# Optimization experiments

Hardware: AMD Instinct MI355X
Metric: run time of the kernel (lower is better)

## Reference

```python
import jax, jax.numpy as jnp
import numpy as np

B, T, D_MODEL = 4, 2048, 1024
D_EXPERT, N_EXPERTS, TOP_K = 4096, 8, 2
CAPACITY_FACTOR = 1.25
AUX_COEFF, Z_COEFF = 0.01, 0.001


def setup_inputs() -> dict:
    key = jax.random.key(0)
    k = jax.random.split(key, 4)
    x = jax.random.normal(k[0], (B, T, D_MODEL), jnp.float32)
    Wr = jax.random.normal(k[1], (D_MODEL, N_EXPERTS), jnp.float32) * 0.02
    W1 = jax.random.normal(k[2], (N_EXPERTS, D_MODEL, D_EXPERT), jnp.float32) * (1.0 / np.sqrt(D_MODEL))
    b1 = jnp.zeros((N_EXPERTS, D_EXPERT), jnp.float32)
    W2 = jax.random.normal(k[3], (N_EXPERTS, D_EXPERT, D_MODEL), jnp.float32) * (1.0 / np.sqrt(D_EXPERT))
    b2 = jnp.zeros((N_EXPERTS, D_MODEL), jnp.float32)
    return {"x": x, "Wr": Wr, "W1": W1, "b1": b1, "W2": W2, "b2": b2}


def reference(x, Wr, W1, b1, W2, b2):
    Bb, Tt, D = x.shape
    N = Bb * Tt
    E = W1.shape[0]
    capacity = max(1, int(N / E * CAPACITY_FACTOR * TOP_K))

    xf = x.reshape(N, D)
    logits = xf @ Wr                                    # (N, E)
    z_loss = jnp.mean(jax.nn.logsumexp(logits, axis=-1) ** 2)
    probs = jax.nn.softmax(logits, axis=-1)             # (N, E)

    topk_p, topk_i = jax.lax.top_k(probs, TOP_K)        # (N, K)
    # one-hot expert mask (top-k experts are distinct per token)
    mask = jnp.zeros((N, E), probs.dtype).at[jnp.arange(N)[:, None], topk_i].set(1.0)

    # capacity truncation: keep first `capacity` assigned tokens per expert, in token order
    pos = (jnp.cumsum(mask, axis=0) - mask).astype(jnp.int32)   # exclusive rank within expert
    keep = (pos < capacity) & (mask > 0)
    mask_t = jnp.where(keep, mask, jnp.zeros_like(mask))

    # Switch-style aux loss on truncated mask
    total_sel = jnp.maximum(mask_t.sum(), 1.0)
    f_i = mask_t.sum(axis=0) / total_sel
    P_i = probs.mean(axis=0)
    aux_loss = E * jnp.sum(f_i * P_i)

    # normalized top-k combine weights (differentiable through probs)
    tk_raw = jnp.take_along_axis(probs, topk_i, axis=1)          # (N, K)
    tk = tk_raw / jnp.maximum(tk_raw.sum(axis=-1, keepdims=True), 1e-9)

    # dispatch tokens into (E, capacity, D) buffer; dropped tokens scatter out of range
    pos_safe = jnp.where(keep, pos, capacity)                    # capacity -> dropped
    pos_k = jnp.take_along_axis(pos_safe, topk_i, axis=1)        # (N, K)
    upd = jnp.broadcast_to(xf[:, None, :], (N, TOP_K, D)).reshape(-1, D)
    buf = jnp.zeros((E, capacity, D), x.dtype).at[topk_i.reshape(-1), pos_k.reshape(-1)].set(upd, mode='drop')

    # grouped expert MLP
    h = jax.nn.relu(jnp.einsum('ecd,edf->ecf', buf, W1) + b1[:, None, :])
    eo = jnp.einsum('ecf,efd->ecd', h, W2) + b2[:, None, :]      # (E, capacity, D)

    # combine: gather each token's top-k expert outputs, weight, sum; dropped -> weight 0
    valid_k = jnp.take_along_axis(keep, topk_i, axis=1)          # (N, K) bool
    w = tk * valid_k.astype(tk.dtype)
    pos_g = jnp.minimum(pos_k, capacity - 1)
    gathered = eo[topk_i, pos_g]                                 # (N, K, D)
    out = jnp.einsum('nk,nkd->nd', w, gathered).reshape(Bb, Tt, D)

    total_aux = AUX_COEFF * aux_loss + Z_COEFF * z_loss
    return out, aux_loss, z_loss, total_aux
```

## Files before the change

kernel.cpp:

```cpp
#include <hip/hip_runtime.h>
#include <stdint.h>

#define N_TOK    8192
#define DM       1024
#define DE       4096
#define NEXP     8
#define CAP      2560
#define AUX_CO   0.01f
#define Z_CO     0.001f

typedef __attribute__((ext_vector_type(4))) float f32x4;
typedef __attribute__((ext_vector_type(8))) __bf16 bf16x8;

static __device__ __forceinline__ unsigned short f2bf(float f) {
  union { float f; uint32_t u; } v; v.f = f;
  uint32_t r = 0x7fffu + ((v.u >> 16) & 1u);
  return (unsigned short)((v.u + r) >> 16);
}
static __device__ __forceinline__ float bf2f(unsigned short u) {
  union { uint32_t u; float f; } v; v.u = ((uint32_t)u) << 16;
  return v.f;
}

#define GLD16(g, l) __builtin_amdgcn_global_load_lds( \
    (const __attribute__((address_space(1))) void*)(g), \
    (__attribute__((address_space(3))) void*)(l), 16, 0, 0)

__global__ void init_inv(int* __restrict__ inv) {
  int i = blockIdx.x * 256 + threadIdx.x;
  if (i < NEXP * CAP) inv[i] = -1;
}

__global__ __launch_bounds__(256) void transpose_to_bf16(
    const float* __restrict__ in, unsigned short* __restrict__ out, int R, int C)
{
  __shared__ float tile[32][33];
  const size_t eoff = (size_t)blockIdx.z * R * C;
  const int bx = blockIdx.x * 32, by = blockIdx.y * 32;
  const int r = threadIdx.x >> 3, c4 = (threadIdx.x & 7) * 4;
  const float4 v = *(const float4*)&in[eoff + (size_t)(by + r) * C + bx + c4];
  tile[r][c4 + 0] = v.x; tile[r][c4 + 1] = v.y;
  tile[r][c4 + 2] = v.z; tile[r][c4 + 3] = v.w;
  __syncthreads();
  const int oc = threadIdx.x >> 3, r4 = (threadIdx.x & 7) * 4;
  ushort4 o;
  o.x = f2bf(tile[r4 + 0][oc]); o.y = f2bf(tile[r4 + 1][oc]);
  o.z = f2bf(tile[r4 + 2][oc]); o.w = f2bf(tile[r4 + 3][oc]);
  *(ushort4*)&out[eoff + (size_t)(bx + oc) * R + by + r4] = o;
}

__global__ __launch_bounds__(256) void router_kernel(
    const float* __restrict__ x, const float* __restrict__ Wr,
    int* __restrict__ topk, float* __restrict__ tkw, float* __restrict__ zP)
{
  const int tid = threadIdx.x, lane = tid & 63, wave = tid >> 6;
  float zacc = 0.f;
  float pacc[NEXP];
#pragma unroll
  for (int e = 0; e < NEXP; ++e) pacc[e] = 0.f;

  for (int it = 0; it < 4; ++it) {
    const int t = blockIdx.x * 16 + it * 4 + wave;
    float acc[NEXP];
#pragma unroll
    for (int e = 0; e < NEXP; ++e) acc[e] = 0.f;
    const f32x4* x4 = (const f32x4*)(x + (size_t)t * DM);
#pragma unroll
    for (int i = 0; i < 4; ++i) {
      f32x4 xv = x4[i * 64 + lane];
#pragma unroll
      for (int j = 0; j < 4; ++j) {
        const float xs = xv[j];
        const float* wr = Wr + (size_t)((i * 64 + lane) * 4 + j) * NEXP;
#pragma unroll
        for (int e = 0; e < NEXP; ++e) acc[e] += xs * wr[e];
      }
    }
#pragma unroll
    for (int m = 32; m; m >>= 1)
#pragma unroll
      for (int e = 0; e < NEXP; ++e) acc[e] += __shfl_xor(acc[e], m);

    float mx = acc[0];
#pragma unroll
    for (int e = 1; e < NEXP; ++e) mx = fmaxf(mx, acc[e]);
    float p[NEXP], s = 0.f;
#pragma unroll
    for (int e = 0; e < NEXP; ++e) { p[e] = expf(acc[e] - mx); s += p[e]; }
    const float lse = mx + logf(s);
    zacc += lse * lse;
    const float inv_s = 1.f / s;
#pragma unroll
    for (int e = 0; e < NEXP; ++e) pacc[e] += p[e] * inv_s;

    int e0 = 0; float v0 = p[0];
#pragma unroll
    for (int e = 1; e < NEXP; ++e) if (p[e] > v0) { v0 = p[e]; e0 = e; }
    int e1 = -1; float v1 = -1.f;
#pragma unroll
    for (int e = 0; e < NEXP; ++e) if (e != e0 && p[e] > v1) { v1 = p[e]; e1 = e; }

    const float pr0 = v0 * inv_s, pr1 = v1 * inv_s;
    const float denom = fmaxf(pr0 + pr1, 1e-9f);
    if (lane == 0) {
      topk[2*t]   = e0; topk[2*t+1] = e1;
      tkw[2*t]    = pr0 / denom; tkw[2*t+1] = pr1 / denom;
    }
  }
  __shared__ float blk[4][9];
  if (lane == 0) {
    blk[wave][0] = zacc;
#pragma unroll
    for (int e = 0; e < NEXP; ++e) blk[wave][1 + e] = pacc[e];
  }
  __syncthreads();
  if (tid < 9)
    zP[blockIdx.x * 9 + tid] = blk[0][tid] + blk[1][tid] + blk[2][tid] + blk[3][tid];
}

__global__ __launch_bounds__(512) void scan_kernel(
    const int2* __restrict__ topk, const float2* __restrict__ tkw,
    int* __restrict__ posk, float* __restrict__ wts,
    int* __restrict__ inv, int* __restrict__ kept)
{
  const int lane = threadIdx.x & 63;
  const int e = threadIdx.x >> 6;
  int base = 0;
  const uint64_t below = (lane == 63) ? 0xFFFFFFFFFFFFFFFFull >> 1
                                      : ((1ull << lane) - 1ull);
  for (int i = 0; i < N_TOK / 64; ++i) {
    const int t = i * 64 + lane;
    const int2 ti = topk[t];
    const float2 w = tkw[t];
    const bool hit = (ti.x == e) || (ti.y == e);
    const uint64_t m = __ballot(hit);
    if (hit) {
      const int pos = base + (int)__popcll(m & below);
      const bool kp = pos < CAP;
      const int k = (ti.x == e) ? 0 : 1;
      posk[2*t + k] = kp ? pos : CAP;
      wts[2*t + k]  = kp ? ((k == 0) ? w.x : w.y) : 0.f;
      if (kp) inv[e * CAP + pos] = t;
    }
    base += (int)__popcll(m);
  }
  if (lane == 0) kept[e] = base < CAP ? base : CAP;
}

__global__ __launch_bounds__(256) void dispatch_kernel(
    const float* __restrict__ x, const int* __restrict__ inv,
    unsigned short* __restrict__ buf)
{
  const int slot = blockIdx.x;
  const int t = inv[slot];
  ushort4 o;
  if (t >= 0) {
    const f32x4 v = ((const f32x4*)(x + (size_t)t * DM))[threadIdx.x];
    o.x = f2bf(v[0]); o.y = f2bf(v[1]); o.z = f2bf(v[2]); o.w = f2bf(v[3]);
  } else {
    o.x = 0; o.y = 0; o.z = 0; o.w = 0;
  }
  ((ushort4*)(buf + (size_t)slot * DM))[threadIdx.x] = o;
}

template<int BM, int BN, bool RELU>
__global__ __launch_bounds__(512, (BM == 256) ? 2 : 4) void gemm2p(
    const unsigned short* __restrict__ A,
    const unsigned short* __restrict__ Bt,
    const float* __restrict__ bias,
    unsigned short* __restrict__ C,
    const int* __restrict__ kept,
    int M, int N, int K, int mt, int nt, int nwg)
{
  constexpr int MF = BM / 32;
  constexpr int NF = BN / 64;
  constexpr int ABUF = BM * 64;
  constexpr int BBUF = BN * 64;
  __shared__ __attribute__((aligned(16))) unsigned short As[2 * ABUF];
  __shared__ __attribute__((aligned(16))) unsigned short Bs[2 * BBUF];

  const int tid = threadIdx.x, lane = tid & 63, wave = tid >> 6;
  const int wr = wave >> 2, wc = wave & 3;
  const int frow = lane & 15, kgrp = lane >> 4;

  int wg = (int)blockIdx.x;
  wg = (wg & 7) * (nwg >> 3) + (wg >> 3);
  const int ntpe = mt * nt;
  const int e = wg / ntpe, rr = wg % ntpe;
  const int m0 = (rr / nt) * BM;
  const int n0 = (rr % nt) * BN;
  if (m0 >= kept[e]) return;

  const unsigned short* Ae = A  + (size_t)e * M * K + (size_t)m0 * K;
  const unsigned short* Be = Bt + (size_t)e * N * K + (size_t)n0 * K;

  const int srow = tid >> 3;
  const int scol = ((tid & 7) ^ (srow & 7)) * 8;

  auto stage = [&](int buf, int k0) {
#pragma unroll
    for (int i = 0; i < BM / 64; ++i)
      GLD16(Ae + (size_t)(i * 64 + srow) * K + (k0 + scol),
            &As[buf * ABUF + i * 4096 + tid * 8]);
#pragma unroll
    for (int i = 0; i < BN / 64; ++i)
      GLD16(Be + (size_t)(i * 64 + srow) * K + (k0 + scol),
            &Bs[buf * BBUF + i * 4096 + tid * 8]);
  };

  f32x4 acc[MF][NF];
#pragma unroll
  for (int m = 0; m < MF; ++m)
#pragma unroll
    for (int n = 0; n < NF; ++n) acc[m][n] = (f32x4){0.f, 0.f, 0.f, 0.f};

  const int nk = K >> 6;
  stage(0, 0);
  for (int t = 0; t < nk; ++t) {
    const int cur = t & 1;
    __syncthreads();
    if (t + 1 < nk) stage(cur ^ 1, (t + 1) * 64);
#pragma unroll
    for (int kk = 0; kk < 2; ++kk) {
      bf16x8 bq[NF], af[MF];
#pragma unroll
      for (int n = 0; n < NF; ++n) {
        const int row = wc * (BN / 4) + n * 16 + frow;
        const int slot = (kk * 4 + kgrp) ^ (row & 7);
        bq[n] = *(const bf16x8*)&Bs[cur * BBUF + row * 64 + slot * 8];
      }
#pragma unroll
      for (int m = 0; m < MF; ++m) {
        const int row = wr * (BM / 2) + m * 16 + frow;
        const int slot = (kk * 4 + kgrp) ^ (row & 7);
        af[m] = *(const bf16x8*)&As[cur * ABUF + row * 64 + slot * 8];
      }
      __builtin_amdgcn_s_setprio(1);
#pragma unroll
      for (int m = 0; m < MF; ++m)
#pragma unroll
        for (int n = 0; n < NF; ++n)
          acc[m][n] = __builtin_amdgcn_mfma_f32_16x16x32_bf16(af[m], bq[n], acc[m][n], 0, 0, 0);
      __builtin_amdgcn_s_setprio(0);
    }
  }

  const int r0 = m0 + wr * (BM / 2) + 4 * kgrp;
  const int c0 = n0 + wc * (BN / 4) + frow;
#pragma unroll
  for (int n = 0; n < NF; ++n) {
    const int cc = c0 + n * 16;
    const float bv = bias[(size_t)e * N + cc];
#pragma unroll
    for (int m = 0; m < MF; ++m) {
#pragma unroll
      for (int r = 0; r < 4; ++r) {
        float v = acc[m][n][r] + bv;
        if (RELU) v = fmaxf(v, 0.f);
        C[((size_t)e * M + (r0 + m * 16 + r)) * N + cc] = f2bf(v);
      }
    }
  }
}

__global__ __launch_bounds__(256) void combine_kernel(
    const unsigned short* __restrict__ eo, const int* __restrict__ posk,
    const float* __restrict__ wts, const int* __restrict__ topk,
    float* __restrict__ out)
{
  const int t = blockIdx.x;
  const int e0 = topk[2*t], e1 = topk[2*t+1];
  int p0 = posk[2*t], p1 = posk[2*t+1];
  p0 = p0 < CAP - 1 ? p0 : CAP - 1;
  p1 = p1 < CAP - 1 ? p1 : CAP - 1;
  const float w0 = wts[2*t], w1 = wts[2*t+1];
  const ushort4 a = ((const ushort4*)(eo + ((size_t)e0 * CAP + p0) * DM))[threadIdx.x];
  const ushort4 b = ((const ushort4*)(eo + ((size_t)e1 * CAP + p1) * DM))[threadIdx.x];
  f32x4 o;
  o[0] = w0 * bf2f(a.x) + w1 * bf2f(b.x);
  o[1] = w0 * bf2f(a.y) + w1 * bf2f(b.y);
  o[2] = w0 * bf2f(a.z) + w1 * bf2f(b.z);
  o[3] = w0 * bf2f(a.w) + w1 * bf2f(b.w);
  ((f32x4*)(out + (size_t)t * DM))[threadIdx.x] = o;
}

__global__ __launch_bounds__(64) void finalize_kernel(
    const float* __restrict__ zP, const int* __restrict__ kept,
    float* __restrict__ outs)
{
  const int lane = threadIdx.x;
  float v[9];
#pragma unroll
  for (int e = 0; e < 9; ++e) {
    float s = 0.f;
    for (int b = 0; b < 8; ++b) s += zP[(lane * 8 + b) * 9 + e];
    v[e] = s;
  }
#pragma unroll
  for (int m = 32; m; m >>= 1)
#pragma unroll
    for (int e = 0; e < 9; ++e) v[e] += __shfl_xor(v[e], m);
  if (lane == 0) {
    const float z = v[0] / (float)N_TOK;
    float total = 0.f;
    for (int e = 0; e < NEXP; ++e) total += (float)kept[e];
    total = fmaxf(total, 1.f);
    float aux = 0.f;
    for (int e = 0; e < NEXP; ++e)
      aux += ((float)kept[e] / total) * (v[1 + e] / (float)N_TOK);
    aux *= (float)NEXP;
    outs[0] = aux;
    outs[1] = z;
    outs[2] = AUX_CO * aux + Z_CO * z;
  }
}

extern "C" void kernel_launch(void* const* d_in, const int* in_sizes, int n_in,
                              void* d_out, int out_size, void* d_ws, size_t ws_size,
                              hipStream_t stream)
{
  const float* x  = (const float*)d_in[0];
  const float* Wr = (const float*)d_in[1];
  const float* W1 = (const float*)d_in[2];
  const float* b1 = (const float*)d_in[3];
  const float* W2 = (const float*)d_in[4];
  const float* b2 = (const float*)d_in[5];
  float* out = (float*)d_out;

  char* p = (char*)d_ws;
  auto alloc = [&](size_t bytes) {
    char* q = p; p += (bytes + 255) & ~(size_t)255; return q;
  };
  unsigned short* W1t = (unsigned short*)alloc((size_t)NEXP * DM * DE * 2);
  unsigned short* W2t = (unsigned short*)alloc((size_t)NEXP * DM * DE * 2);
  unsigned short* buf = (unsigned short*)alloc((size_t)NEXP * CAP * DM * 2);
  unsigned short* h   = (unsigned short*)alloc((size_t)NEXP * CAP * DE * 2);
  unsigned short* eo  = (unsigned short*)alloc((size_t)NEXP * CAP * DM * 2);
  int*   topk = (int*)alloc((size_t)N_TOK * 2 * 4);
  float* tkw  = (float*)alloc((size_t)N_TOK * 2 * 4);
  int*   posk = (int*)alloc((size_t)N_TOK * 2 * 4);
  float* wts  = (float*)alloc((size_t)N_TOK * 2 * 4);
  int*   inv  = (int*)alloc((size_t)NEXP * CAP * 4);
  int*   kept = (int*)alloc((size_t)NEXP * 4);
  float* zP   = (float*)alloc((size_t)512 * 9 * 4);

  init_inv<<<(NEXP * CAP + 255) / 256, 256, 0, stream>>>(inv);
  transpose_to_bf16<<<dim3(DE / 32, DM / 32, NEXP), 256, 0, stream>>>(W1, W1t, DM, DE);
  transpose_to_bf16<<<dim3(DM / 32, DE / 32, NEXP), 256, 0, stream>>>(W2, W2t, DE, DM);
  router_kernel<<<512, 256, 0, stream>>>(x, Wr, topk, tkw, zP);
  scan_kernel<<<1, 512, 0, stream>>>((const int2*)topk, (const float2*)tkw, posk, wts, inv, kept);
  dispatch_kernel<<<NEXP * CAP, 256, 0, stream>>>(x, inv, buf);

  gemm2p<256, 256, true><<<1280, 512, 0, stream>>>(
      buf, W1t, b1, h, kept, CAP, DE, DM, 10, 16, 1280);
  gemm2p<128, 128, false><<<1280, 512, 0, stream>>>(
      h, W2t, b2, eo, kept, CAP, DM, DE, 20, 8, 1280);

  combine_kernel<<<N_TOK, 256, 0, stream>>>(eo, posk, wts, topk, out);
  finalize_kernel<<<1, 64, 0, stream>>>(zP, kept, out + (size_t)N_TOK * DM);
}
```

Before: 651.1 us.

## Add hand-scheduled 8-phase pipelined GEMM for first expert layer and fold inv init into scan

Replaces the first expert GEMM with a new 256x256 kernel that splits each K-step into four MFMA quadrants, interleaving LDS reads and async global-to-LDS loads between them with explicit waitcnt, barriers and priority hints. The aim is to overlap memory traffic with MFMA work more tightly. The scan kernel now stages topk and weights in shared memory and fills the unused inv slots itself, which removes the separate init kernel launch. The manual scheduling is fragile and depends on exact vmcnt counts being correct.

```diff
diff --git a/kernel.cpp b/kernel.cpp
--- a/kernel.cpp
+++ b/kernel.cpp
@@ -22,14 +22,15 @@
   return v.f;
 }
 
+#define MEMFENCE() asm volatile("" ::: "memory")
+#define BAR()    do { MEMFENCE(); __builtin_amdgcn_s_barrier(); MEMFENCE(); } while (0)
+#define LGKM0()  asm volatile("s_waitcnt lgkmcnt(0)" ::: "memory")
+#define LGKM8()  asm volatile("s_waitcnt lgkmcnt(8)" ::: "memory")
+#define VMW(N)   asm volatile("s_waitcnt vmcnt(" #N ")" ::: "memory")
+#define SB0()    __builtin_amdgcn_sched_barrier(0)
 #define GLD16(g, l) __builtin_amdgcn_global_load_lds( \
     (const __attribute__((address_space(1))) void*)(g), \
     (__attribute__((address_space(3))) void*)(l), 16, 0, 0)
-
-__global__ void init_inv(int* __restrict__ inv) {
-  int i = blockIdx.x * 256 + threadIdx.x;
-  if (i < NEXP * CAP) inv[i] = -1;
-}
 
 __global__ __launch_bounds__(256) void transpose_to_bf16(
     const float* __restrict__ in, unsigned short* __restrict__ out, int R, int C)
@@ -123,15 +124,21 @@
     int* __restrict__ posk, float* __restrict__ wts,
     int* __restrict__ inv, int* __restrict__ kept)
 {
-  const int lane = threadIdx.x & 63;
-  const int e = threadIdx.x >> 6;
+  __shared__ int2   stopk[N_TOK];
+  __shared__ float2 stkw[N_TOK];
+  const int tid = threadIdx.x;
+  for (int j = tid; j < N_TOK; j += 512) { stopk[j] = topk[j]; stkw[j] = tkw[j]; }
+  __syncthreads();
+
+  const int lane = tid & 63;
+  const int e = tid >> 6;
   int base = 0;
   const uint64_t below = (lane == 63) ? 0xFFFFFFFFFFFFFFFFull >> 1
                                       : ((1ull << lane) - 1ull);
   for (int i = 0; i < N_TOK / 64; ++i) {
     const int t = i * 64 + lane;
-    const int2 ti = topk[t];
-    const float2 w = tkw[t];
+    const int2 ti = stopk[t];
+    const float2 w = stkw[t];
     const bool hit = (ti.x == e) || (ti.y == e);
     const uint64_t m = __ballot(hit);
     if (hit) {
@@ -144,7 +151,9 @@
     }
     base += (int)__popcll(m);
   }
-  if (lane == 0) kept[e] = base < CAP ? base : CAP;
+  const int tail = base < CAP ? base : CAP;
+  for (int q = tail + lane; q < CAP; q += 64) inv[e * CAP + q] = -1;
+  if (lane == 0) kept[e] = tail;
 }
 
 __global__ __launch_bounds__(256) void dispatch_kernel(
@@ -256,6 +265,147 @@
 #pragma unroll
       for (int r = 0; r < 4; ++r) {
         float v = acc[m][n][r] + bv;
+        if (RELU) v = fmaxf(v, 0.f);
+        C[((size_t)e * M + (r0 + m * 16 + r)) * N + cc] = f2bf(v);
+      }
+    }
+  }
+}
+
+template<bool RELU>
+__global__ __launch_bounds__(512, 2) void gemm8p(
+    const unsigned short* __restrict__ A,
+    const unsigned short* __restrict__ Bt,
+    const float* __restrict__ bias,
+    unsigned short* __restrict__ C,
+    const int* __restrict__ kept,
+    int M, int N, int K, int mt, int nt, int nwg)
+{
+  __shared__ __attribute__((aligned(16))) unsigned short As[2 * 16384];
+  __shared__ __attribute__((aligned(16))) unsigned short Bs[2 * 16384];
+  const int tid = threadIdx.x, lane = tid & 63, wave = tid >> 6;
+  const int wr = wave >> 2, wc = wave & 3;
+  const int frow = lane & 15, kgrp = lane >> 4;
+
+  int wg = (int)blockIdx.x;
+  wg = (wg & 7) * (nwg >> 3) + (wg >> 3);
+  const int ntpe = mt * nt;
+  const int e = wg / ntpe, rr = wg % ntpe;
+  const int m0 = (rr / nt) * 256;
+  const int n0 = (rr % nt) * 256;
+  if (m0 >= kept[e]) return;
+
+  const unsigned short* Ae = A  + (size_t)e * M * K + (size_t)m0 * K;
+  const unsigned short* Be = Bt + (size_t)e * N * K + (size_t)n0 * K;
+
+  const int srow = tid >> 3;
+  const int scol = ((tid & 7) ^ (srow & 7)) * 8;
+
+  auto stA = [&](int t, int h) {
+    const int c = t & 1, k0 = t * 64;
+#pragma unroll
+    for (int i = 0; i < 2; ++i)
+      GLD16(Ae + (size_t)(h * 128 + i * 64 + srow) * K + (k0 + scol),
+            &As[c * 16384 + (h * 128 + i * 64) * 64 + tid * 8]);
+  };
+  auto stB = [&](int t, int h) {
+    const int c = t & 1, k0 = t * 64;
+#pragma unroll
+    for (int i = 0; i < 2; ++i)
+      GLD16(Be + (size_t)(h * 128 + i * 64 + srow) * K + (k0 + scol),
+            &Bs[c * 16384 + (h * 128 + i * 64) * 64 + tid * 8]);
+  };
+  auto rdA = [&](bf16x8* dst, int c, int mh) {
+#pragma unroll
+    for (int m = 0; m < 4; ++m) {
+      const int row = wr * 128 + mh * 64 + m * 16 + frow;
+#pragma unroll
+      for (int kk = 0; kk < 2; ++kk)
+        dst[m * 2 + kk] = *(const bf16x8*)
+          &As[c * 16384 + row * 64 + (((kk * 4 + kgrp) ^ (row & 7)) * 8)];
+    }
+  };
+  auto rdB = [&](bf16x8* dst, int c, int nh) {
+#pragma unroll
+    for (int n = 0; n < 2; ++n) {
+      const int row = wc * 64 + nh * 32 + n * 16 + frow;
+#pragma unroll
+      for (int kk = 0; kk < 2; ++kk)
+        dst[n * 2 + kk] = *(const bf16x8*)
+          &Bs[c * 16384 + row * 64 + (((kk * 4 + kgrp) ^ (row & 7)) * 8)];
+    }
+  };
+
+  f32x4 acc[8][4];
+#pragma unroll
+  for (int m = 0; m < 8; ++m)
+#pragma unroll
+    for (int n = 0; n < 4; ++n) acc[m][n] = (f32x4){0.f, 0.f, 0.f, 0.f};
+
+  bf16x8 af0[8], af1[8], bq0[4], bq1[4];
+  auto mfmaQ = [&](int mh, int nh, bf16x8* af, bf16x8* bq) {
+#pragma unroll
+    for (int m = 0; m < 4; ++m)
+#pragma unroll
+      for (int n = 0; n < 2; ++n)
+#pragma unroll
+        for (int kk = 0; kk < 2; ++kk)
+          acc[mh * 4 + m][nh * 2 + n] = __builtin_amdgcn_mfma_f32_16x16x32_bf16(
+              af[m * 2 + kk], bq[n * 2 + kk], acc[mh * 4 + m][nh * 2 + n], 0, 0, 0);
+  };
+
+  const int nk = K >> 6;
+
+  stA(0, 0); stA(0, 1); stB(0, 0); stB(0, 1);
+  stA(1, 0); stA(1, 1); stB(1, 0);
+  VMW(6);
+  BAR();
+
+  for (int t = 0; t < nk; ++t) {
+    const int c = t & 1;
+    rdA(af0, c, 0);
+    rdB(bq0, c, 0);
+    if (t + 1 < nk) stB(t + 1, 1);
+    LGKM8();
+    BAR(); LGKM0(); SB0();
+    __builtin_amdgcn_s_setprio(1);
+    mfmaQ(0, 0, af0, bq0);
+    __builtin_amdgcn_s_setprio(0);
+    BAR();
+    rdA(af1, c, 1);
+    BAR(); LGKM0(); SB0();
+    __builtin_amdgcn_s_setprio(1);
+    mfmaQ(1, 0, af1, bq0);
+    __builtin_amdgcn_s_setprio(0);
+    BAR();
+    rdB(bq1, c, 1);
+    if (t + 2 < nk) stA(t + 2, 0);
+    BAR(); LGKM0(); SB0();
+    __builtin_amdgcn_s_setprio(1);
+    mfmaQ(0, 1, af0, bq1);
+    __builtin_amdgcn_s_setprio(0);
+    BAR();
+    if (t + 2 < nk) { stA(t + 2, 1); stB(t + 2, 0); }
+    BAR(); SB0();
+    __builtin_amdgcn_s_setprio(1);
+    mfmaQ(1, 1, af1, bq1);
+    __builtin_amdgcn_s_setprio(0);
+    if (t + 2 < nk)      { VMW(6); }
+    else if (t + 1 < nk) { VMW(0); }
+    if (t + 1 < nk) BAR();
+  }
+
+  const int r0 = m0 + wr * 128 + 4 * kgrp;
+  const int c0 = n0 + wc * 64 + frow;
+#pragma unroll
+  for (int nf = 0; nf < 4; ++nf) {
+    const int cc = c0 + nf * 16;
+    const float bv = bias[(size_t)e * N + cc];
+#pragma unroll
+    for (int m = 0; m < 8; ++m) {
+#pragma unroll
+      for (int r = 0; r < 4; ++r) {
+        float v = acc[m][nf][r] + bv;
         if (RELU) v = fmaxf(v, 0.f);
         C[((size_t)e * M + (r0 + m * 16 + r)) * N + cc] = f2bf(v);
       }
@@ -344,15 +494,13 @@
   int*   kept = (int*)alloc((size_t)NEXP * 4);
   float* zP   = (float*)alloc((size_t)512 * 9 * 4);
 
-  init_inv<<<(NEXP * CAP + 255) / 256, 256, 0, stream>>>(inv);
   transpose_to_bf16<<<dim3(DE / 32, DM / 32, NEXP), 256, 0, stream>>>(W1, W1t, DM, DE);
   transpose_to_bf16<<<dim3(DM / 32, DE / 32, NEXP), 256, 0, stream>>>(W2, W2t, DE, DM);
   router_kernel<<<512, 256, 0, stream>>>(x, Wr, topk, tkw, zP);
   scan_kernel<<<1, 512, 0, stream>>>((const int2*)topk, (const float2*)tkw, posk, wts, inv, kept);
   dispatch_kernel<<<NEXP * CAP, 256, 0, stream>>>(x, inv, buf);
 
-  gemm2p<256, 256, true><<<1280, 512, 0, stream>>>(
-      buf, W1t, b1, h, kept, CAP, DE, DM, 10, 16, 1280);
+  gemm8p<true><<<1280, 512, 0, stream>>>(buf, W1t, b1, h, kept, CAP, DE, DM, 10, 16, 1280);
   gemm2p<128, 128, false><<<1280, 512, 0, stream>>>(
       h, W2t, b2, eo, kept, CAP, DM, DE, 20, 8, 1280);
 
```

New measurement: 592.7 us. 9.0% less time.
